# Performance work log

Hardware: AMD Instinct MI355X
Metric: run time of the kernel (lower is better)

The kernel has to match this reference:

```python
import jax, jax.numpy as jnp
import numpy as np

N = 50000
E = 800000
NODE_IN = 128
HID = 256
OUT = 256
EDGE_DIM = 16
HEADS = 4
CH = HID // HEADS  # 64
NEG_SLOPE = 0.2


def _init_linear(key, fan_in, fan_out):
    k1, k2 = jax.random.split(key)
    bound = 1.0 / np.sqrt(fan_in)
    W = jax.random.uniform(k1, (fan_in, fan_out), jnp.float32, -bound, bound)
    b = jax.random.uniform(k2, (fan_out,), jnp.float32, -bound, bound)
    return W, b


def setup_inputs() -> dict:
    key = jax.random.key(0)
    ks = jax.random.split(key, 12)
    node_feats = jax.random.normal(ks[0], (N, NODE_IN), jnp.float32)
    edge_index = jax.random.randint(ks[1], (2, E), 0, N, jnp.int64)
    edge_attr = jax.random.normal(ks[2], (E, EDGE_DIM), jnp.float32)

    Wnp, bnp = _init_linear(ks[3], NODE_IN, HID)           # node_proj
    Wep, bep = _init_linear(ks[4], EDGE_DIM, HID)          # edge_proj
    # GATConv 1: in = 2*HID, out per head = CH
    Wg1, _ = _init_linear(ks[5], 2 * HID, HEADS * CH)
    as1 = jax.random.normal(ks[6], (HEADS, CH), jnp.float32) * 0.1
    ad1 = jax.random.normal(ks[7], (HEADS, CH), jnp.float32) * 0.1
    bg1 = jnp.zeros((HEADS * CH,), jnp.float32)
    # GATConv 2: in = HID, out per head = OUT//HEADS
    Wg2, _ = _init_linear(ks[8], HID, HEADS * (OUT // HEADS))
    as2 = jax.random.normal(ks[9], (HEADS, OUT // HEADS), jnp.float32) * 0.1
    ad2 = jax.random.normal(ks[10], (HEADS, OUT // HEADS), jnp.float32) * 0.1
    bg2 = jnp.zeros((OUT,), jnp.float32)
    Wo, bo = _init_linear(ks[11], OUT, OUT)                # out_proj
    return {
        "node_feats": node_feats, "edge_attr": edge_attr,
        "Wnp": Wnp, "bnp": bnp, "Wep": Wep, "bep": bep,
        "Wg1": Wg1, "as1": as1, "ad1": ad1, "bg1": bg1,
        "Wg2": Wg2, "as2": as2, "ad2": ad2, "bg2": bg2,
        "Wo": Wo, "bo": bo,
        "edge_index": edge_index,
    }


def scatter_mean(src, index, num_nodes):
    # mean of edge features grouped by target node; empty groups -> 0 (count clamped to 1)
    s = jax.ops.segment_sum(src, index, num_segments=num_nodes)
    cnt = jax.ops.segment_sum(jnp.ones((src.shape[0],), src.dtype), index, num_segments=num_nodes)
    return s / jnp.maximum(cnt, 1.0)[:, None]


def gat_conv(x, src, dst, W, att_src, att_dst, bias, num_nodes, heads, ch):
    # PyG GATConv with add_self_loops=True (loops appended by caller via src/dst),
    # concat=True, negative_slope=0.2.
    xh = (x @ W).reshape(num_nodes, heads, ch)             # [N,H,C]
    a_src = jnp.sum(xh * att_src, axis=-1)                 # [N,H]
    a_dst = jnp.sum(xh * att_dst, axis=-1)                 # [N,H]
    logits = jax.nn.leaky_relu(a_src[src] + a_dst[dst], NEG_SLOPE)  # [E,H]
    # segment softmax over incoming edges of each destination node
    m = jax.ops.segment_max(logits, dst, num_segments=num_nodes)    # [N,H]
    ex = jnp.exp(logits - m[dst])
    denom = jax.ops.segment_sum(ex, dst, num_segments=num_nodes)    # [N,H]
    alpha = ex / denom[dst]                                          # [E,H]
    msg = xh[src] * alpha[:, :, None]                                # [E,H,C]
    out = jax.ops.segment_sum(msg, dst, num_segments=num_nodes)      # [N,H,C]
    return out.reshape(num_nodes, heads * ch) + bias


def reference(node_feats, edge_attr, Wnp, bnp, Wep, bep,
              Wg1, as1, ad1, bg1, Wg2, as2, ad2, bg2, Wo, bo, edge_index):
    n = node_feats.shape[0]
    x = node_feats @ Wnp + bnp                                       # [N,HID]
    # EdgeAggregator: mean of edge_attr over target nodes, then edge_proj
    nef = scatter_mean(edge_attr, edge_index[1], n)                  # [N,EDGE_DIM]
    nef = nef @ Wep + bep                                            # [N,HID]
    x = jnp.concatenate([x, nef], axis=-1)                           # [N,2*HID]
    # add self loops once (same augmented edge set for both GAT layers)
    loops = jnp.arange(n, dtype=edge_index.dtype)
    src = jnp.concatenate([edge_index[0], loops])
    dst = jnp.concatenate([edge_index[1], loops])
    x = jax.nn.elu(gat_conv(x, src, dst, Wg1, as1, ad1, bg1, n, HEADS, CH))
    # dropout is identity in eval mode
    x = jax.nn.elu(gat_conv(x, src, dst, Wg2, as2, ad2, bg2, n, HEADS, OUT // HEADS))
    return x @ Wo + bo
```

## Files before the change

### kernel.cpp

```cpp
#include <hip/hip_runtime.h>
#include <hip/hip_bf16.h>


#define HEADS 4

typedef __attribute__((ext_vector_type(8))) short bf16x8;
typedef __attribute__((ext_vector_type(4))) float f32x4;
typedef __attribute__((ext_vector_type(4))) unsigned short u16x4;

__device__ __forceinline__ unsigned short f2b(float v) {
    __hip_bfloat16 b = __float2bfloat16(v);
    return __builtin_bit_cast(unsigned short, b);
}
__device__ __forceinline__ float b2f(unsigned short u) {
    __hip_bfloat16 b = __builtin_bit_cast(__hip_bfloat16, u);
    return __bfloat162float(b);
}
__device__ __forceinline__ void split_hilo(float v, unsigned short& h, unsigned short& l) {
    h = f2b(v);
    l = f2b(v - b2f(h));
}
__device__ __forceinline__ unsigned short f2h(float v) {
    _Float16 h = (_Float16)v;
    return __builtin_bit_cast(unsigned short, h);
}
__device__ __forceinline__ float h2f(unsigned short u) {
    return (float)__builtin_bit_cast(_Float16, u);
}
__device__ __forceinline__ void gl2lds16(const unsigned short* g, unsigned short* l) {
    __builtin_amdgcn_global_load_lds(
        (const __attribute__((address_space(1))) unsigned int*)g,
        (__attribute__((address_space(3))) unsigned int*)l,
        16, 0, 0);
}


__global__ __launch_bounds__(256) void count_kernel(
    const int* __restrict__ dst, int* __restrict__ cnt, int E)
{
    int e = blockIdx.x * 256 + threadIdx.x;
    if (e < E) atomicAdd(&cnt[dst[e]], 1);
}

__global__ __launch_bounds__(256) void scan1_kernel(
    const int* __restrict__ cnt, int* __restrict__ chunk_sum, int N)
{
    __shared__ int sd[256];
    int t = threadIdx.x;
    int n = blockIdx.x * 256 + t;
    sd[t] = (n < N) ? (cnt[n] + 1) : 0;
    __syncthreads();
    for (int o = 128; o > 0; o >>= 1) {
        if (t < o) sd[t] += sd[t + o];
        __syncthreads();
    }
    if (t == 0) chunk_sum[blockIdx.x] = sd[0];
}

__global__ void scan2_kernel(const int* __restrict__ chunk_sum,
                             int* __restrict__ chunk_off, int nchunk)
{
    int acc = 0;
    for (int i = 0; i < nchunk; i++) {
        chunk_off[i] = acc;
        acc += chunk_sum[i];
    }
}

__global__ __launch_bounds__(256) void scan3_kernel(
    const int* __restrict__ cnt, const int* __restrict__ chunk_off,
    int* __restrict__ rowptr, int* __restrict__ fillptr,
    int* __restrict__ col, int* __restrict__ eid, int N)
{
    __shared__ int sd[256];
    int t = threadIdx.x;
    int n = blockIdx.x * 256 + t;
    int v = (n < N) ? (cnt[n] + 1) : 0;
    sd[t] = v;
    __syncthreads();
    for (int o = 1; o < 256; o <<= 1) {
        int x = (t >= o) ? sd[t - o] : 0;
        __syncthreads();
        sd[t] += x;
        __syncthreads();
    }
    if (n < N) {
        int incl = sd[t];
        int r = chunk_off[blockIdx.x] + incl - v;
        rowptr[n] = r;
        col[r] = n;
        eid[r] = -1;
        fillptr[n] = r + 1;
        if (n == N - 1) rowptr[N] = chunk_off[blockIdx.x] + incl;
    }
}

__global__ __launch_bounds__(256) void fill_kernel(
    const int* __restrict__ src, const int* __restrict__ dst,
    int* __restrict__ fillptr, int* __restrict__ col, int* __restrict__ eid, int E)
{
    int e = blockIdx.x * 256 + threadIdx.x;
    if (e >= E) return;
    int d = dst[e];
    int p = atomicAdd(&fillptr[d], 1);
    col[p] = src[e];
    eid[p] = e;
}

__global__ __launch_bounds__(256) void nef_csr_kernel(
    const float* __restrict__ ea, const int* __restrict__ rowptr,
    const int* __restrict__ eid,
    unsigned short* __restrict__ AH, unsigned short* __restrict__ AL, int N)
{
    int n = blockIdx.x * 4 + (threadIdx.x >> 6);
    if (n >= N) return;
    int t = threadIdx.x & 63;
    int f = t & 15, g = t >> 4;
    int base = rowptr[n], end = rowptr[n + 1];
    int deg = end - base - 1;
    float acc = 0.0f;
    for (int j = base + 1 + g; j < end; j += 4) {
        int e = eid[j];
        acc += ea[(size_t)e * 16 + f];
    }
    acc += __shfl_down(acc, 32, 64);
    acc += __shfl_down(acc, 16, 64);
    if (t < 16) {
        float v = acc / fmaxf((float)deg, 1.0f);
        unsigned short h, l;
        split_hilo(v, h, l);
        AH[(size_t)n * 160 + 128 + t] = h;
        AL[(size_t)n * 160 + 128 + t] = l;
    } else if (t < 32) {
        AH[(size_t)n * 160 + 128 + t] = 0;
        AL[(size_t)n * 160 + 128 + t] = 0;
    }
}

__global__ __launch_bounds__(256) void conv_hilo_strided_kernel(
    const float* __restrict__ X,
    unsigned short* __restrict__ H, unsigned short* __restrict__ L, int total)
{
    int base = (blockIdx.x * 256 + threadIdx.x) * 2;
    if (base >= total) return;
    #pragma unroll
    for (int i = 0; i < 2; i++) {
        int e = base + i;
        int row = e >> 7, c = e & 127;
        unsigned short h, l;
        split_hilo(X[e], h, l);
        H[(size_t)row * 160 + c] = h;
        L[(size_t)row * 160 + c] = l;
    }
}

__global__ __launch_bounds__(256) void compose_w1_kernel(
    const float* __restrict__ Wnp, const float* __restrict__ Wep,
    const float* __restrict__ bnp, const float* __restrict__ bep,
    const float* __restrict__ Wg1,
    float* __restrict__ Wc, float* __restrict__ c1)
{
    int idx = blockIdx.x * 256 + threadIdx.x;
    if (idx >= 145 * 256) return;
    int i = idx >> 8, j = idx & 255;
    float s = 0.0f;
    if (i < 128) {
        for (int k = 0; k < 256; k++) s += Wnp[i * 256 + k] * Wg1[(size_t)k * 256 + j];
        Wc[i * 256 + j] = s;
    } else if (i < 144) {
        int ii = i - 128;
        for (int k = 0; k < 256; k++) s += Wep[ii * 256 + k] * Wg1[(size_t)(256 + k) * 256 + j];
        Wc[i * 256 + j] = s;
    } else {
        for (int k = 0; k < 256; k++)
            s += bnp[k] * Wg1[(size_t)k * 256 + j] + bep[k] * Wg1[(size_t)(256 + k) * 256 + j];
        c1[j] = s;
    }
}

__global__ __launch_bounds__(256) void pack_w_kernel(
    const float* __restrict__ W, int K, int KP,
    unsigned short* __restrict__ Ph, unsigned short* __restrict__ Pl)
{
    int idx = blockIdx.x * 256 + threadIdx.x;
    if (idx >= KP * 256) return;
    int tile = idx >> 9, w = idx & 511, lane = w >> 3, j = w & 7;
    int nk = KP >> 5;
    int ctile = tile / nk, t = tile % nk;
    int k = t * 32 + ((lane >> 4) << 3) + j;
    int n = (ctile << 4) + (lane & 15);
    float v = (k < K) ? W[(size_t)k * 256 + n] : 0.0f;
    unsigned short h, l;
    split_hilo(v, h, l);
    Ph[idx] = h;
    Pl[idx] = l;
}

template <int KSTEPS, int OMODE, bool FUSE_ATT>
__global__ __launch_bounds__(256, 5) void mfma_gemm_kernel(
    const unsigned short* __restrict__ Ah, const unsigned short* __restrict__ Al,
    int lda,
    const unsigned short* __restrict__ Ph, const unsigned short* __restrict__ Pl,
    const float* __restrict__ bias,
    float* __restrict__ Cf,
    unsigned short* __restrict__ Ch, unsigned short* __restrict__ Cl,
    int ldc, int col_off, int Nrows,
    const float* __restrict__ att_src, const float* __restrict__ att_dst,
    float* __restrict__ a_srcO, float* __restrict__ a_dstO)
{
    __shared__ unsigned short ldsB[2][2][8][512];
    int tid = threadIdx.x;
    int wave = tid >> 6, lane = tid & 63;
    int quad = lane >> 4, m16 = lane & 15;
    int rowblk = blockIdx.x, colhalf = blockIdx.y;
    int ctile0 = colhalf * 8;

    int row = rowblk * 64 + wave * 16 + m16;
    bool rowok = row < Nrows;
    const unsigned short* arh = Ah + (size_t)row * lda;
    const unsigned short* arl = Al + (size_t)row * lda;

    auto stage = [&](int t, int buf) {
        #pragma unroll
        for (int q = 0; q < 2; q++) {
            int c = wave * 2 + q;
            size_t gb = ((size_t)((ctile0 + c) * KSTEPS + t)) * 512 + lane * 8;
            gl2lds16(Ph + gb, &ldsB[buf][0][c][0]);
            gl2lds16(Pl + gb, &ldsB[buf][1][c][0]);
        }
    };

    f32x4 acc[8] = {};
    stage(0, 0);
    __syncthreads();

    for (int t = 0; t < KSTEPS; t++) {
        const int buf = t & 1;
        if (t + 1 < KSTEPS) stage(t + 1, buf ^ 1);
        int k = t * 32 + quad * 8;
        bf16x8 a_h = {}, a_l = {};
        if (rowok) {
            a_h = *(const bf16x8*)(arh + k);
            a_l = *(const bf16x8*)(arl + k);
        }
        #pragma unroll
        for (int c = 0; c < 8; c++) {
            bf16x8 b_h = *(const bf16x8*)&ldsB[buf][0][c][lane * 8];
            bf16x8 b_l = *(const bf16x8*)&ldsB[buf][1][c][lane * 8];
            acc[c] = __builtin_amdgcn_mfma_f32_16x16x32_bf16(a_h, b_h, acc[c], 0, 0, 0);
            acc[c] = __builtin_amdgcn_mfma_f32_16x16x32_bf16(a_l, b_h, acc[c], 0, 0, 0);
            acc[c] = __builtin_amdgcn_mfma_f32_16x16x32_bf16(a_h, b_l, acc[c], 0, 0, 0);
        }
        if (t + 1 < KSTEPS) __syncthreads();
    }

    #pragma unroll
    for (int c = 0; c < 8; c++) {
        int ocol = (ctile0 + c) * 16 + m16;
        float bv = bias ? bias[ocol] : 0.0f;
        #pragma unroll
        for (int r = 0; r < 4; r++) {
            int orow = rowblk * 64 + wave * 16 + quad * 4 + r;
            if (orow >= Nrows) continue;
            float v = acc[c][r] + bv;
            size_t oidx = (size_t)orow * ldc + col_off + ocol;
            if (OMODE == 1) {
                unsigned short h, l;
                split_hilo(v, h, l);
                Ch[oidx] = h;
                Cl[oidx] = l;
            } else if (OMODE == 2) {
                Ch[oidx] = f2h(v);
            } else {
                Cf[oidx] = v;
            }
        }
    }

    if (FUSE_ATT) {
        float ps[4][2] = {}, pd[4][2] = {};
        #pragma unroll
        for (int c = 0; c < 8; c++) {
            int ocol = (ctile0 + c) * 16 + m16;
            float bv = bias ? bias[ocol] : 0.0f;
            float asv = att_src[ocol];
            float adv = att_dst[ocol];
            int hl = c >> 2;
            #pragma unroll
            for (int r = 0; r < 4; r++) {
                float v = acc[c][r] + bv;
                ps[r][hl] += v * asv;
                pd[r][hl] += v * adv;
            }
        }
        #pragma unroll
        for (int r = 0; r < 4; r++) {
            #pragma unroll
            for (int hl = 0; hl < 2; hl++) {
                float s = ps[r][hl], d = pd[r][hl];
                #pragma unroll
                for (int o = 8; o > 0; o >>= 1) {
                    s += __shfl_down(s, o, 64);
                    d += __shfl_down(d, o, 64);
                }
                if (m16 == 0) {
                    int orow = rowblk * 64 + wave * 16 + quad * 4 + r;
                    if (orow < Nrows) {
                        int gh = colhalf * 2 + hl;
                        a_srcO[orow * 4 + gh] = s;
                        a_dstO[orow * 4 + gh] = d;
                    }
                }
            }
        }
    }
}

__global__ __launch_bounds__(256) void edge_w_kernel(
    const int* __restrict__ rowptr, const int* __restrict__ col,
    const float* __restrict__ a_src, const float* __restrict__ a_dst,
    float* __restrict__ wq, float* __restrict__ den, int N)
{
    int n = blockIdx.x * 4 + (threadIdx.x >> 6);
    if (n >= N) return;
    int lane = threadIdx.x & 63;
    int base = rowptr[n], end = rowptr[n + 1];
    float4 ad = *(const float4*)&a_dst[n * 4];
    float4 ds = {0.0f, 0.0f, 0.0f, 0.0f};
    for (int j = base + lane; j < end; j += 64) {
        int s = col[j];
        float4 as4 = *(const float4*)&a_src[s * 4];
        float l0 = as4.x + ad.x, l1 = as4.y + ad.y;
        float l2 = as4.z + ad.z, l3 = as4.w + ad.w;
        l0 = fmaxf(l0, 0.2f * l0);
        l1 = fmaxf(l1, 0.2f * l1);
        l2 = fmaxf(l2, 0.2f * l2);
        l3 = fmaxf(l3, 0.2f * l3);
        float4 wv = {__expf(l0), __expf(l1), __expf(l2), __expf(l3)};
        *(float4*)&wq[(size_t)j * 4] = wv;
        ds.x += wv.x; ds.y += wv.y; ds.z += wv.z; ds.w += wv.w;
    }
    #pragma unroll
    for (int o = 32; o > 0; o >>= 1) {
        ds.x += __shfl_down(ds.x, o, 64);
        ds.y += __shfl_down(ds.y, o, 64);
        ds.z += __shfl_down(ds.z, o, 64);
        ds.w += __shfl_down(ds.w, o, 64);
    }
    if (lane == 0) *(float4*)&den[n * 4] = ds;
}

__global__ __launch_bounds__(256) void gat_agg_csr_kernel(
    const unsigned short* __restrict__ xh,
    const int* __restrict__ rowptr, const int* __restrict__ col,
    const float* __restrict__ wq, const float* __restrict__ den,
    const float* __restrict__ bias,
    unsigned short* __restrict__ outH, unsigned short* __restrict__ outL, int N)
{
    int t = threadIdx.x;
    int n = blockIdx.x * 4 + (t >> 6);
    if (n >= N) return;
    int c = t & 63;
    int h = c >> 4;
    int base = rowptr[n], end = rowptr[n + 1];
    int e1 = end - 1;
    float inv = 1.0f / den[n * 4 + h];
    const unsigned short* xcol = xh + (c << 2);

    float4 acc = {0.0f, 0.0f, 0.0f, 0.0f};
    for (int j = base; j < end; j += 4) {
        int j1 = j + 1 < e1 ? j + 1 : e1;
        int j2 = j + 2 < e1 ? j + 2 : e1;
        int j3 = j + 3 < e1 ? j + 3 : e1;
        int s0 = col[j], s1 = col[j1], s2 = col[j2], s3 = col[j3];
        float w0 = wq[(size_t)j * 4 + h];
        float w1 = (j + 1 < end) ? wq[(size_t)j1 * 4 + h] : 0.0f;
        float w2 = (j + 2 < end) ? wq[(size_t)j2 * 4 + h] : 0.0f;
        float w3 = (j + 3 < end) ? wq[(size_t)j3 * 4 + h] : 0.0f;
        u16x4 x0 = *(const u16x4*)(xcol + (size_t)s0 * 256);
        u16x4 x1 = *(const u16x4*)(xcol + (size_t)s1 * 256);
        u16x4 x2 = *(const u16x4*)(xcol + (size_t)s2 * 256);
        u16x4 x3 = *(const u16x4*)(xcol + (size_t)s3 * 256);
        acc.x += w0 * h2f(x0[0]) + w1 * h2f(x1[0]) + w2 * h2f(x2[0]) + w3 * h2f(x3[0]);
        acc.y += w0 * h2f(x0[1]) + w1 * h2f(x1[1]) + w2 * h2f(x2[1]) + w3 * h2f(x3[1]);
        acc.z += w0 * h2f(x0[2]) + w1 * h2f(x1[2]) + w2 * h2f(x2[2]) + w3 * h2f(x3[2]);
        acc.w += w0 * h2f(x0[3]) + w1 * h2f(x1[3]) + w2 * h2f(x2[3]) + w3 * h2f(x3[3]);
    }

    float4 bv = *(const float4*)(bias + (c << 2));
    float o0 = acc.x * inv + bv.x;
    float o1 = acc.y * inv + bv.y;
    float o2 = acc.z * inv + bv.z;
    float o3 = acc.w * inv + bv.w;
    o0 = (o0 > 0.0f) ? o0 : (__expf(o0) - 1.0f);
    o1 = (o1 > 0.0f) ? o1 : (__expf(o1) - 1.0f);
    o2 = (o2 > 0.0f) ? o2 : (__expf(o2) - 1.0f);
    o3 = (o3 > 0.0f) ? o3 : (__expf(o3) - 1.0f);
    u16x4 H, L;
    split_hilo(o0, ((unsigned short*)&H)[0], ((unsigned short*)&L)[0]);
    split_hilo(o1, ((unsigned short*)&H)[1], ((unsigned short*)&L)[1]);
    split_hilo(o2, ((unsigned short*)&H)[2], ((unsigned short*)&L)[2]);
    split_hilo(o3, ((unsigned short*)&H)[3], ((unsigned short*)&L)[3]);
    *(u16x4*)(&outH[(size_t)n * 256 + (c << 2)]) = H;
    *(u16x4*)(&outL[(size_t)n * 256 + (c << 2)]) = L;
}


extern "C" void kernel_launch(void* const* d_in, const int* in_sizes, int n_in,
                              void* d_out, int out_size, void* d_ws, size_t ws_size,
                              hipStream_t stream)
{
    const float* node_feats = (const float*)d_in[0];
    const float* edge_attr  = (const float*)d_in[1];
    const float* Wnp = (const float*)d_in[2];
    const float* bnp = (const float*)d_in[3];
    const float* Wep = (const float*)d_in[4];
    const float* bep = (const float*)d_in[5];
    const float* Wg1 = (const float*)d_in[6];
    const float* as1 = (const float*)d_in[7];
    const float* ad1 = (const float*)d_in[8];
    const float* bg1 = (const float*)d_in[9];
    const float* Wg2 = (const float*)d_in[10];
    const float* as2 = (const float*)d_in[11];
    const float* ad2 = (const float*)d_in[12];
    const float* bg2 = (const float*)d_in[13];
    const float* Wo  = (const float*)d_in[14];
    const float* bo  = (const float*)d_in[15];
    const int*   ei  = (const int*)d_in[16];

    const int N = in_sizes[0] / 128;
    const int E = in_sizes[16] / 2;
    const int* src = ei;
    const int* dst = ei + E;
    const int nchunk = (N + 255) / 256;
    const int EN = E + N;

    typedef unsigned short u16;

    char* base = (char*)d_ws;
    size_t off = 0;
    auto alloc = [&](size_t bytes) -> char* {
        char* p = base + off;
        off += (bytes + 255) & ~(size_t)255;
        return p;
    };
    u16* xhh = (u16*)alloc((size_t)N * 256 * 2);
    u16* R2  = (u16*)alloc((size_t)N * 512 * 2);
    u16* R3  = (u16*)alloc((size_t)N * 512 * 2);
    float* a_src = (float*)alloc((size_t)N * 4 * 4);
    float* a_dst = (float*)alloc((size_t)N * 4 * 4);
    float* wq    = (float*)alloc((size_t)EN * 4 * 4);
    float* den   = (float*)alloc((size_t)N * 4 * 4);
    float* Wc    = (float*)alloc(144 * 256 * 4);
    float* c1    = (float*)alloc(256 * 4);
    u16* PcH  = (u16*)alloc(160 * 256 * 2);
    u16* PcL  = (u16*)alloc(160 * 256 * 2);
    u16* Pg2H = (u16*)alloc(256 * 256 * 2);
    u16* Pg2L = (u16*)alloc(256 * 256 * 2);
    u16* PoH  = (u16*)alloc(256 * 256 * 2);
    u16* PoL  = (u16*)alloc(256 * 256 * 2);
    int* cnt       = (int*)alloc((size_t)N * 4);
    int* rowptr    = (int*)alloc((size_t)(N + 1) * 4);
    int* fillptr   = (int*)alloc((size_t)N * 4);
    int* chunk_sum = (int*)alloc((size_t)nchunk * 4);
    int* chunk_off = (int*)alloc((size_t)nchunk * 4);
    int* colv      = (int*)alloc((size_t)EN * 4);
    int* eid       = (int*)alloc((size_t)EN * 4);

    u16* AcatH = R2;
    u16* AcatL = R3;
    u16* x3H = R2;
    u16* x3L = R2 + (size_t)N * 256;
    u16* x4H = R3;
    u16* x4L = R3 + (size_t)N * 256;

    float* out = (float*)d_out;
    dim3 ggrid((N + 63) / 64, 2);

    hipMemsetAsync(cnt, 0, (size_t)N * sizeof(int), stream);
    count_kernel<<<(E + 255) / 256, 256, 0, stream>>>(dst, cnt, E);
    scan1_kernel<<<nchunk, 256, 0, stream>>>(cnt, chunk_sum, N);
    scan2_kernel<<<1, 1, 0, stream>>>(chunk_sum, chunk_off, nchunk);
    scan3_kernel<<<nchunk, 256, 0, stream>>>(cnt, chunk_off, rowptr, fillptr, colv, eid, N);
    fill_kernel<<<(E + 255) / 256, 256, 0, stream>>>(src, dst, fillptr, colv, eid, E);

    nef_csr_kernel<<<(N + 3) / 4, 256, 0, stream>>>(edge_attr, rowptr, eid, AcatH, AcatL, N);
    conv_hilo_strided_kernel<<<((N * 128) / 2 + 255) / 256, 256, 0, stream>>>(
        node_feats, AcatH, AcatL, N * 128);
    compose_w1_kernel<<<145, 256, 0, stream>>>(Wnp, Wep, bnp, bep, Wg1, Wc, c1);
    pack_w_kernel<<<(160 * 256 + 255) / 256, 256, 0, stream>>>(Wc, 144, 160, PcH, PcL);
    pack_w_kernel<<<(256 * 256 + 255) / 256, 256, 0, stream>>>(Wg2, 256, 256, Pg2H, Pg2L);
    pack_w_kernel<<<(256 * 256 + 255) / 256, 256, 0, stream>>>(Wo, 256, 256, PoH, PoL);

    mfma_gemm_kernel<5, 2, true><<<ggrid, 256, 0, stream>>>(
        AcatH, AcatL, 160, PcH, PcL, c1, nullptr, xhh, nullptr, 256, 0, N,
        as1, ad1, a_src, a_dst);
    edge_w_kernel<<<(N + 3) / 4, 256, 0, stream>>>(
        rowptr, colv, a_src, a_dst, wq, den, N);
    gat_agg_csr_kernel<<<(N + 3) / 4, 256, 0, stream>>>(
        xhh, rowptr, colv, wq, den, bg1, x3H, x3L, N);

    mfma_gemm_kernel<8, 2, true><<<ggrid, 256, 0, stream>>>(
        x3H, x3L, 256, Pg2H, Pg2L, nullptr, nullptr, xhh, nullptr, 256, 0, N,
        as2, ad2, a_src, a_dst);
    edge_w_kernel<<<(N + 3) / 4, 256, 0, stream>>>(
        rowptr, colv, a_src, a_dst, wq, den, N);
    gat_agg_csr_kernel<<<(N + 3) / 4, 256, 0, stream>>>(
        xhh, rowptr, colv, wq, den, bg2, x4H, x4L, N);

    mfma_gemm_kernel<8, 0, false><<<ggrid, 256, 0, stream>>>(
        x4H, x4L, 256, PoH, PoL, bo, out, nullptr, nullptr, 256, 0, N,
        nullptr, nullptr, nullptr, nullptr);
}
```

Before: 584.1 us.

## Parallelize chunk scan, merge weight packing launches, prefetch A fragments in GEMM

Replaces the single-thread serial chunk-offset scan with a 256-thread block scan. Merges the three weight-packing launches into one kernel to cut launch overhead. In the MFMA GEMM, the A-row fragments for the next k-step are loaded into double-buffered registers alongside the B staging, so global loads overlap the MFMAs. The GEMM change raises register pressure under a 5-blocks-per-CU launch bound.

```diff
diff --git a/kernel.cpp b/kernel.cpp
--- a/kernel.cpp
+++ b/kernel.cpp
@@ -57,13 +57,29 @@
     if (t == 0) chunk_sum[blockIdx.x] = sd[0];
 }
 
-__global__ void scan2_kernel(const int* __restrict__ chunk_sum,
-                             int* __restrict__ chunk_off, int nchunk)
-{
-    int acc = 0;
-    for (int i = 0; i < nchunk; i++) {
-        chunk_off[i] = acc;
-        acc += chunk_sum[i];
+__global__ __launch_bounds__(256) void scan2_kernel(
+    const int* __restrict__ chunk_sum, int* __restrict__ chunk_off, int nchunk)
+{
+    __shared__ int sd[256];
+    __shared__ int carry;
+    int t = threadIdx.x;
+    if (t == 0) carry = 0;
+    __syncthreads();
+    for (int b = 0; b < nchunk; b += 256) {
+        int i = b + t;
+        int v = (i < nchunk) ? chunk_sum[i] : 0;
+        sd[t] = v;
+        __syncthreads();
+        for (int o = 1; o < 256; o <<= 1) {
+            int x = (t >= o) ? sd[t - o] : 0;
+            __syncthreads();
+            sd[t] += x;
+            __syncthreads();
+        }
+        if (i < nchunk) chunk_off[i] = carry + sd[t] - v;
+        __syncthreads();
+        if (t == 0) carry += sd[255];
+        __syncthreads();
     }
 }
 
@@ -178,12 +194,10 @@
     }
 }
 
-__global__ __launch_bounds__(256) void pack_w_kernel(
-    const float* __restrict__ W, int K, int KP,
+__device__ __forceinline__ void pack_one(
+    const float* __restrict__ W, int K, int KP, int idx,
     unsigned short* __restrict__ Ph, unsigned short* __restrict__ Pl)
 {
-    int idx = blockIdx.x * 256 + threadIdx.x;
-    if (idx >= KP * 256) return;
     int tile = idx >> 9, w = idx & 511, lane = w >> 3, j = w & 7;
     int nk = KP >> 5;
     int ctile = tile / nk, t = tile % nk;
@@ -194,6 +208,24 @@
     split_hilo(v, h, l);
     Ph[idx] = h;
     Pl[idx] = l;
+}
+
+__global__ __launch_bounds__(256) void pack3_w_kernel(
+    const float* __restrict__ Wc,  unsigned short* __restrict__ PcH,  unsigned short* __restrict__ PcL,
+    const float* __restrict__ Wg2, unsigned short* __restrict__ Pg2H, unsigned short* __restrict__ Pg2L,
+    const float* __restrict__ Wo,  unsigned short* __restrict__ PoH,  unsigned short* __restrict__ PoL)
+{
+    const int S0 = 160 * 256;
+    const int S1 = S0 + 256 * 256;
+    const int S2 = S1 + 256 * 256;
+    int idx = blockIdx.x * 256 + threadIdx.x;
+    if (idx < S0) {
+        pack_one(Wc, 144, 160, idx, PcH, PcL);
+    } else if (idx < S1) {
+        pack_one(Wg2, 256, 256, idx - S0, Pg2H, Pg2L);
+    } else if (idx < S2) {
+        pack_one(Wo, 256, 256, idx - S1, PoH, PoL);
+    }
 }
 
 template <int KSTEPS, int OMODE, bool FUSE_ATT>
@@ -229,27 +261,36 @@
             gl2lds16(Pl + gb, &ldsB[buf][1][c][0]);
         }
     };
+    auto loadA = [&](int t, bf16x8& h, bf16x8& l) {
+        int k = t * 32 + quad * 8;
+        h = (bf16x8){};
+        l = (bf16x8){};
+        if (rowok) {
+            h = *(const bf16x8*)(arh + k);
+            l = *(const bf16x8*)(arl + k);
+        }
+    };
 
     f32x4 acc[8] = {};
+    bf16x8 ah2[2], al2[2];
+    loadA(0, ah2[0], al2[0]);
     stage(0, 0);
     __syncthreads();
 
+    #pragma unroll
     for (int t = 0; t < KSTEPS; t++) {
         const int buf = t & 1;
-        if (t + 1 < KSTEPS) stage(t + 1, buf ^ 1);
-        int k = t * 32 + quad * 8;
-        bf16x8 a_h = {}, a_l = {};
-        if (rowok) {
-            a_h = *(const bf16x8*)(arh + k);
-            a_l = *(const bf16x8*)(arl + k);
+        if (t + 1 < KSTEPS) {
+            stage(t + 1, buf ^ 1);
+            loadA(t + 1, ah2[(t + 1) & 1], al2[(t + 1) & 1]);
         }
         #pragma unroll
         for (int c = 0; c < 8; c++) {
             bf16x8 b_h = *(const bf16x8*)&ldsB[buf][0][c][lane * 8];
             bf16x8 b_l = *(const bf16x8*)&ldsB[buf][1][c][lane * 8];
-            acc[c] = __builtin_amdgcn_mfma_f32_16x16x32_bf16(a_h, b_h, acc[c], 0, 0, 0);
-            acc[c] = __builtin_amdgcn_mfma_f32_16x16x32_bf16(a_l, b_h, acc[c], 0, 0, 0);
-            acc[c] = __builtin_amdgcn_mfma_f32_16x16x32_bf16(a_h, b_l, acc[c], 0, 0, 0);
+            acc[c] = __builtin_amdgcn_mfma_f32_16x16x32_bf16(ah2[buf], b_h, acc[c], 0, 0, 0);
+            acc[c] = __builtin_amdgcn_mfma_f32_16x16x32_bf16(al2[buf], b_h, acc[c], 0, 0, 0);
+            acc[c] = __builtin_amdgcn_mfma_f32_16x16x32_bf16(ah2[buf], b_l, acc[c], 0, 0, 0);
         }
         if (t + 1 < KSTEPS) __syncthreads();
     }
@@ -480,7 +521,7 @@
     hipMemsetAsync(cnt, 0, (size_t)N * sizeof(int), stream);
     count_kernel<<<(E + 255) / 256, 256, 0, stream>>>(dst, cnt, E);
     scan1_kernel<<<nchunk, 256, 0, stream>>>(cnt, chunk_sum, N);
-    scan2_kernel<<<1, 1, 0, stream>>>(chunk_sum, chunk_off, nchunk);
+    scan2_kernel<<<1, 256, 0, stream>>>(chunk_sum, chunk_off, nchunk);
     scan3_kernel<<<nchunk, 256, 0, stream>>>(cnt, chunk_off, rowptr, fillptr, colv, eid, N);
     fill_kernel<<<(E + 255) / 256, 256, 0, stream>>>(src, dst, fillptr, colv, eid, E);
 
@@ -488,9 +529,11 @@
     conv_hilo_strided_kernel<<<((N * 128) / 2 + 255) / 256, 256, 0, stream>>>(
         node_feats, AcatH, AcatL, N * 128);
     compose_w1_kernel<<<145, 256, 0, stream>>>(Wnp, Wep, bnp, bep, Wg1, Wc, c1);
-    pack_w_kernel<<<(160 * 256 + 255) / 256, 256, 0, stream>>>(Wc, 144, 160, PcH, PcL);
-    pack_w_kernel<<<(256 * 256 + 255) / 256, 256, 0, stream>>>(Wg2, 256, 256, Pg2H, Pg2L);
-    pack_w_kernel<<<(256 * 256 + 255) / 256, 256, 0, stream>>>(Wo, 256, 256, PoH, PoL);
+    {
+        const int total = 160 * 256 + 256 * 256 + 256 * 256;
+        pack3_w_kernel<<<(total + 255) / 256, 256, 0, stream>>>(
+            Wc, PcH, PcL, Wg2, Pg2H, Pg2L, Wo, PoH, PoL);
+    }
 
     mfma_gemm_kernel<5, 2, true><<<ggrid, 256, 0, stream>>>(
         AcatH, AcatL, 160, PcH, PcL, c1, nullptr, xhh, nullptr, 256, 0, N,
```

Result: faster. 571.5 us (-2.2%).
